# Optimization experiments

Measured on AMD Instinct MI355X. Metric: run time of the kernel, lower is better.

The kernel has to match this reference:

```python
import jax, jax.numpy as jnp
import numpy as np

D_MODEL, D_STATE, EXPAND, D_CONV, HEADDIM = 1024, 128, 2, 4, 64
D_INNER = EXPAND * D_MODEL                      # 2048
NHEADS = D_INNER // HEADDIM                     # 32
NGROUPS = 1
CONV_DIM = D_INNER + 2 * NGROUPS * D_STATE      # 2304
D_IN_PROJ = 2 * D_INNER + 2 * NGROUPS * D_STATE + NHEADS  # 4384
BATCH, SEQ = 2, 4096
EPS = 1e-5


def setup_inputs() -> dict:
    key = jax.random.key(0)
    ks = jax.random.split(key, 6)
    sn = lambda k, shape, sc: jax.random.normal(k, shape, jnp.float32) * sc
    # dt_bias such that softplus(dt_bias) spans [1e-3, 0.1] (mamba2 init)
    dt = jnp.linspace(1e-3, 0.1, NHEADS)
    return {
        "x": sn(ks[0], (BATCH, SEQ, D_MODEL), 1.0),
        "ln_w": jnp.ones((D_MODEL,), jnp.float32),
        "ln_b": jnp.zeros((D_MODEL,), jnp.float32),
        "in_proj_w": sn(ks[1], (D_IN_PROJ, D_MODEL), D_MODEL ** -0.5),
        "conv_w": sn(ks[2], (CONV_DIM, D_CONV), D_CONV ** -0.5),
        "conv_b": jnp.zeros((CONV_DIM,), jnp.float32),
        "dt_bias": jnp.log(jnp.expm1(dt)).astype(jnp.float32),
        "A_log": jnp.log(jnp.arange(1, NHEADS + 1, dtype=jnp.float32)),
        "D": jnp.ones((NHEADS,), jnp.float32),
        "norm_w": jnp.ones((D_INNER,), jnp.float32),
        "out_proj_w": sn(ks[3], (D_MODEL, D_INNER), D_INNER ** -0.5),
    }


def _mamba2(u, in_proj_w, conv_w, conv_b, dt_bias, A_log, Dp, norm_w, out_proj_w):
    b, l, _ = u.shape
    zxbcdt = u @ in_proj_w.T                              # [b,l,4384]
    z, xBC, dt = jnp.split(zxbcdt, [D_INNER, D_INNER + CONV_DIM], axis=-1)
    # causal depthwise conv1d over channels, then SiLU
    xBC = jnp.transpose(xBC, (0, 2, 1))                   # [b,conv_dim,l]
    xBC = jax.lax.conv_general_dilated(
        xBC, conv_w[:, None, :], window_strides=(1,),
        padding=[(D_CONV - 1, 0)], feature_group_count=CONV_DIM,
        dimension_numbers=("NCH", "OIH", "NCH"))
    xBC = jax.nn.silu(jnp.transpose(xBC, (0, 2, 1)) + conv_b)
    x, Bm, Cm = jnp.split(xBC, [D_INNER, D_INNER + NGROUPS * D_STATE], axis=-1)
    dt = jax.nn.softplus(dt + dt_bias)                    # [b,l,h]
    A = -jnp.exp(A_log)                                   # [h]
    xh = x.reshape(b, l, NHEADS, HEADDIM)
    # time-major for the selective scan
    dt_t, x_t = jnp.moveaxis(dt, 1, 0), jnp.moveaxis(xh, 1, 0)
    B_t, C_t = jnp.moveaxis(Bm, 1, 0), jnp.moveaxis(Cm, 1, 0)

    def step(h, inputs):
        dtk, xk, Bk, Ck = inputs                          # [b,h],[b,h,p],[b,n],[b,n]
        decay = jnp.exp(dtk * A)                          # [b,h]
        h = h * decay[:, :, None, None] + (dtk[:, :, None, None] * xk[..., None]) * Bk[:, None, None, :]
        y = jnp.einsum("bhpn,bn->bhp", h, Ck)
        return h, y

    h0 = jnp.zeros((b, NHEADS, HEADDIM, D_STATE), u.dtype)
    _, ys = jax.lax.scan(step, h0, (dt_t, x_t, B_t, C_t))  # ys: [l,b,h,p]
    y = jnp.moveaxis(ys, 0, 1) + Dp[None, None, :, None] * xh
    y = y.reshape(b, l, D_INNER)
    # gated RMSNorm: rmsnorm(y * silu(z)) * norm_w
    y = y * jax.nn.silu(z)
    y = y * jax.lax.rsqrt(jnp.mean(y * y, axis=-1, keepdims=True) + EPS) * norm_w
    return y @ out_proj_w.T


def reference(x, ln_w, ln_b, in_proj_w, conv_w, conv_b, dt_bias, A_log, D, norm_w, out_proj_w):
    mu = jnp.mean(x, -1, keepdims=True)
    var = jnp.mean((x - mu) ** 2, -1, keepdims=True)
    xn = (x - mu) * jax.lax.rsqrt(var + EPS) * ln_w + ln_b
    # dropout is identity at inference
    return x + _mamba2(xn, in_proj_w, conv_w, conv_b, dt_bias, A_log, D, norm_w, out_proj_w)
```

## Files before the change

kernel.cpp:

```cpp
#include <hip/hip_runtime.h>
#include <cstdint>

#define D_MODEL 1024
#define D_INNER 2048
#define NHEADS 32
#define HEADDIM 64
#define D_STATE 128
#define CONV_DIM 2304
#define D_IN_PROJ 4384
#define SEQ 4096
#define NROWS 8192
#define NPROJ_PAD 4480
#define TCH 128
#define NCHUNK 32
#define CR 8

typedef float f32x4 __attribute__((ext_vector_type(4)));
typedef __bf16 bf16x8 __attribute__((ext_vector_type(8)));
typedef unsigned short u16;

__device__ __forceinline__ u16 f2bf(float f) {
  uint32_t u = __builtin_bit_cast(uint32_t, f);
  u += 0x7FFFu + ((u >> 16) & 1u);
  return (u16)(u >> 16);
}
__device__ __forceinline__ float bf2f(u16 h) {
  return __builtin_bit_cast(float, (uint32_t)h << 16);
}
__device__ __forceinline__ float dexp(float a) { return expf(fminf(0.f, a)); }
__device__ __forceinline__ int sw(int v) { return (((v & 7) ^ ((v >> 3) & 7)) << 3); }

typedef __attribute__((address_space(1))) const void gv_t;
typedef __attribute__((address_space(3))) void lv_t;
__device__ __forceinline__ void gload_lds16(const void* g, void* l) {
  __builtin_amdgcn_global_load_lds((gv_t*)g, (lv_t*)l, 16, 0, 0);
}

__global__ __launch_bounds__(256) void cvt_pad(const float* __restrict__ s,
                                               u16* __restrict__ d, int n_src, int n_dst) {
  int i = (blockIdx.x * 256 + threadIdx.x) * 4;
  int stride = gridDim.x * 256 * 4;
  for (; i < n_dst; i += stride) {
    ushort4 o;
    if (i < n_src) {
      float4 v = *(const float4*)&s[i];
      o.x = f2bf(v.x); o.y = f2bf(v.y); o.z = f2bf(v.z); o.w = f2bf(v.w);
    } else {
      o.x = o.y = o.z = o.w = 0;
    }
    *(ushort4*)&d[i] = o;
  }
}

__global__ __launch_bounds__(256) void cvt_w2s(const float* __restrict__ s,
                                               const float* __restrict__ nw,
                                               u16* __restrict__ d, int n) {
  int i = (blockIdx.x * 256 + threadIdx.x) * 4;
  int stride = gridDim.x * 256 * 4;
  for (; i < n; i += stride) {
    float4 v = *(const float4*)&s[i];
    int c = i & (D_INNER - 1);
    ushort4 o;
    o.x = f2bf(v.x * nw[c]);
    o.y = f2bf(v.y * nw[c + 1]);
    o.z = f2bf(v.z * nw[c + 2]);
    o.w = f2bf(v.w * nw[c + 3]);
    *(ushort4*)&d[i] = o;
  }
}

__global__ __launch_bounds__(256) void ln_kernel(const float* __restrict__ x,
                                                 const float* __restrict__ w,
                                                 const float* __restrict__ b,
                                                 u16* __restrict__ out) {
  int row = blockIdx.x, tid = threadIdx.x;
  const float4 v = *(const float4*)&x[(long)row * D_MODEL + tid * 4];
  float s1 = v.x + v.y + v.z + v.w;
  float s2 = v.x * v.x + v.y * v.y + v.z * v.z + v.w * v.w;
#pragma unroll
  for (int m = 32; m >= 1; m >>= 1) {
    s1 += __shfl_xor(s1, m);
    s2 += __shfl_xor(s2, m);
  }
  __shared__ float p1[4], p2[4];
  if ((tid & 63) == 0) { p1[tid >> 6] = s1; p2[tid >> 6] = s2; }
  __syncthreads();
  s1 = p1[0] + p1[1] + p1[2] + p1[3];
  s2 = p2[0] + p2[1] + p2[2] + p2[3];
  float mean = s1 * (1.f / D_MODEL);
  float var = s2 * (1.f / D_MODEL) - mean * mean;
  float rstd = rsqrtf(var + 1e-5f);
  const float4 wv = *(const float4*)&w[tid * 4];
  const float4 bv = *(const float4*)&b[tid * 4];
  ushort4 o;
  o.x = f2bf((v.x - mean) * rstd * wv.x + bv.x);
  o.y = f2bf((v.y - mean) * rstd * wv.y + bv.y);
  o.z = f2bf((v.z - mean) * rstd * wv.z + bv.z);
  o.w = f2bf((v.w - mean) * rstd * wv.w + bv.w);
  *(ushort4*)&out[(long)row * D_MODEL + tid * 4] = o;
}

template <int MODE>
__global__ __launch_bounds__(256, 4) void gemm_bt(const u16* __restrict__ A,
                                                  const u16* __restrict__ B, int K,
                                                  u16* __restrict__ zb,
                                                  u16* __restrict__ xb,
                                                  float* __restrict__ dtb,
                                                  float* __restrict__ C,
                                                  const float* __restrict__ resid,
                                                  const float* __restrict__ rvec) {
  __shared__ __align__(16) u16 As[128 * 64];
  __shared__ __align__(16) u16 Bs[128 * 64];
  const int tid = threadIdx.x;
  int m0, n0;
  if (MODE == 0) {
    const int k = (blockIdx.x & 7) * 280 + (blockIdx.x >> 3);
    const int st = k / 40, inner = k % 40;
    m0 = ((st & 7) * 8 + (inner & 7)) * 128;
    n0 = ((st >> 3) * 5 + (inner >> 3)) * 128;
  } else {
    const int wg = (blockIdx.x & 7) * 64 + (blockIdx.x >> 3);
    m0 = (wg & 63) * 128;
    n0 = (wg >> 6) * 128;
  }
  const int w = tid >> 6, l = tid & 63;
  const int wm = w >> 1, wn = w & 1;

  f32x4 acc[4][4] = {};

  for (int k0 = 0; k0 < K; k0 += 64) {
#pragma unroll
    for (int i = 0; i < 4; ++i) {
      int idx = i * 256 + tid;
      int row = idx >> 3, slot = idx & 7;
      int ks = slot ^ (row & 7);
      const u16* ga = A + (long)(m0 + row) * K + k0 + ks * 8;
      gload_lds16(ga, (char*)As + idx * 16);
      const u16* gb = B + (long)(n0 + row) * K + k0 + ks * 8;
      gload_lds16(gb, (char*)Bs + idx * 16);
    }
    __syncthreads();
    bf16x8 af[2][4], bfr[2][4];
#pragma unroll
    for (int kk = 0; kk < 2; ++kk)
#pragma unroll
      for (int f = 0; f < 4; ++f) {
        int rowa = wm * 64 + f * 16 + (l & 15);
        int ca = ((kk << 2) | (l >> 4)) ^ (rowa & 7);
        af[kk][f] = *(const bf16x8*)((const char*)As + rowa * 128 + ca * 16);
        int rowb = wn * 64 + f * 16 + (l & 15);
        int cb2 = ((kk << 2) | (l >> 4)) ^ (rowb & 7);
        bfr[kk][f] = *(const bf16x8*)((const char*)Bs + rowb * 128 + cb2 * 16);
      }
#pragma unroll
    for (int kk = 0; kk < 2; ++kk)
#pragma unroll
      for (int mf = 0; mf < 4; ++mf)
#pragma unroll
        for (int nf = 0; nf < 4; ++nf)
          acc[mf][nf] = __builtin_amdgcn_mfma_f32_16x16x32_bf16(
              af[kk][mf], bfr[kk][nf], acc[mf][nf], 0, 0, 0);
    __syncthreads();
  }
#pragma unroll
  for (int mf = 0; mf < 4; ++mf)
#pragma unroll
    for (int nf = 0; nf < 4; ++nf) {
      int col = n0 + wn * 64 + nf * 16 + (l & 15);
#pragma unroll
      for (int r = 0; r < 4; ++r) {
        int rowm = m0 + wm * 64 + mf * 16 + (l >> 4) * 4 + r;
        float v = acc[mf][nf][r];
        if (MODE == 0) {
          if (col < D_INNER)
            zb[(long)rowm * D_INNER + col] = f2bf(v);
          else if (col < D_INNER + CONV_DIM)
            xb[(long)rowm * CONV_DIM + (col - D_INNER)] = f2bf(v);
          else if (col < D_IN_PROJ)
            dtb[(long)rowm * NHEADS + (col - D_INNER - CONV_DIM)] = v;
        } else {
          long off = (long)rowm * D_MODEL + col;
          C[off] = v * rvec[rowm] + resid[off];
        }
      }
    }
}

__global__ __launch_bounds__(256) void conv_silu_kernel(const u16* __restrict__ xr,
                                                        const float* __restrict__ cw,
                                                        const float* __restrict__ cb,
                                                        u16* __restrict__ xp,
                                                        u16* __restrict__ bc) {
  const int c = blockIdx.x * 256 + threadIdx.x;
  const int row0 = blockIdx.y * CR;
  const int t0 = row0 & (SEQ - 1);
  const float4 wv = *(const float4*)&cw[c * 4];
  const float bias = cb[c];
  float xwin[CR + 3];
#pragma unroll
  for (int k = 0; k < CR + 3; ++k) {
    int t = t0 - 3 + k;
    xwin[k] = (t >= 0) ? bf2f(xr[(long)(row0 - 3 + k) * CONV_DIM + c]) : 0.f;
  }
#pragma unroll
  for (int j = 0; j < CR; ++j) {
    float a = bias + xwin[j] * wv.x + xwin[j + 1] * wv.y + xwin[j + 2] * wv.z +
              xwin[j + 3] * wv.w;
    a = a / (1.f + expf(-a));
    int row = row0 + j;
    if (c < D_INNER)
      xp[(long)row * D_INNER + c] = f2bf(a);
    else
      bc[(long)row * (2 * D_STATE) + (c - D_INNER)] = f2bf(a);
  }
}

__global__ __launch_bounds__(256, 3) void ssd_state_kernel(
    const u16* __restrict__ xp, const u16* __restrict__ bcb,
    const float* __restrict__ dtf, const float* __restrict__ dt_bias,
    const float* __restrict__ A_log, u16* __restrict__ S,
    float* __restrict__ cdk) {
  const int hh = blockIdx.x, cc = blockIdx.y, bb = blockIdx.z;
  const int tid = threadIdx.x, w = tid >> 6, l = tid & 63;
  __shared__ __align__(16) u16 BT[128 * 128];
  __shared__ __align__(16) u16 WXT[64 * 128];
  __shared__ float ws[128];
  const long rowbase = (long)bb * SEQ + cc * TCH;
  const float Ah = -expf(A_log[hh]);
  const float dbias = dt_bias[hh];

#pragma unroll
  for (int i = 0; i < 8; ++i) {
    int slot = i * 256 + tid, t = slot >> 4, nb = slot & 15;
    bf16x8 v = *(const bf16x8*)&bcb[(rowbase + t) * 256 + nb * 8];
    const u16* e = (const u16*)&v;
#pragma unroll
    for (int j = 0; j < 8; ++j) {
      int n = nb * 8 + j;
      BT[n * 128 + (t ^ sw(n))] = e[j];
    }
  }
  if (w == 0) {
    float r0 = dtf[(rowbase + l) * NHEADS + hh] + dbias;
    float r1 = dtf[(rowbase + 64 + l) * NHEADS + hh] + dbias;
    float d0 = r0 > 20.f ? r0 : log1pf(expf(r0));
    float d1 = r1 > 20.f ? r1 : log1pf(expf(r1));
    float a0 = d0 * Ah, a1 = d1 * Ah;
#pragma unroll
    for (int d = 1; d < 64; d <<= 1) { float u = __shfl_up(a0, d); if (l >= d) a0 += u; }
#pragma unroll
    for (int d = 1; d < 64; d <<= 1) { float u = __shfl_up(a1, d); if (l >= d) a1 += u; }
    float t0 = __shfl(a0, 63);
    float tot = __shfl(a1, 63) + t0;
    ws[l] = dexp(tot - a0) * d0;
    ws[64 + l] = dexp(tot - (a1 + t0)) * d1;
    if (l == 0) cdk[(bb * 32 + hh) * NCHUNK + cc] = dexp(tot);
  }
  __syncthreads();
#pragma unroll
  for (int i = 0; i < 4; ++i) {
    int slot = i * 256 + tid, t = slot >> 3, pb = slot & 7;
    bf16x8 v = *(const bf16x8*)&xp[(rowbase + t) * D_INNER + hh * 64 + pb * 8];
    float wt = ws[t];
    const u16* e = (const u16*)&v;
#pragma unroll
    for (int j = 0; j < 8; ++j) {
      int p = pb * 8 + j;
      WXT[p * 128 + (t ^ sw(p))] = f2bf(bf2f(e[j]) * wt);
    }
  }
  __syncthreads();

  f32x4 acc[8] = {};
  const int p = w * 16 + (l & 15);
  const int swp = sw(p);
#pragma unroll
  for (int kc = 0; kc < 4; ++kc) {
    int tsl = kc * 32 + (l >> 4) * 8;
    bf16x8 af = *(const bf16x8*)&WXT[p * 128 + (tsl ^ swp)];
#pragma unroll
    for (int nt = 0; nt < 8; ++nt) {
      int n = nt * 16 + (l & 15);
      bf16x8 bfv = *(const bf16x8*)&BT[n * 128 + (tsl ^ sw(n))];
      acc[nt] = __builtin_amdgcn_mfma_f32_16x16x32_bf16(af, bfv, acc[nt], 0, 0, 0);
    }
  }
  u16* Sb = S + ((long)(bb * 32 + hh) * NCHUNK + cc) * 8192;
#pragma unroll
  for (int nt = 0; nt < 8; ++nt)
#pragma unroll
    for (int r = 0; r < 4; ++r) {
      int prow = w * 16 + (l >> 4) * 4 + r;
      Sb[prow * 128 + nt * 16 + (l & 15)] = f2bf(acc[nt][r]);
    }
}

__global__ __launch_bounds__(256) void ssd_combine(u16* __restrict__ SH,
                                                   const float* __restrict__ cdk) {
  const int hh = blockIdx.y, bb = blockIdx.z;
  const int pp = blockIdx.x * 16 + (threadIdx.x >> 4);
  const int nn = (threadIdx.x & 15) * 8;
  const int bh = bb * 32 + hh;
  u16* base = SH + (long)bh * NCHUNK * 8192 + pp * 128 + nn;
  const float* ck = cdk + bh * NCHUNK;
  float h[8] = {};
  for (int c = 0; c < NCHUNK; ++c) {
    bf16x8 sv = *(bf16x8*)(base + (long)c * 8192);
    const u16* se = (const u16*)&sv;
    u16 o[8];
#pragma unroll
    for (int j = 0; j < 8; ++j) o[j] = f2bf(h[j]);
    *(bf16x8*)(base + (long)c * 8192) = *(bf16x8*)o;
    float d = ck[c];
#pragma unroll
    for (int j = 0; j < 8; ++j) h[j] = fmaf(h[j], d, bf2f(se[j]));
  }
}

__global__ __launch_bounds__(256, 2) void ssd_y_kernel(
    const u16* __restrict__ xp, const u16* __restrict__ bcb,
    const float* __restrict__ dtf, const float* __restrict__ dt_bias,
    const float* __restrict__ A_log, const float* __restrict__ Dp,
    const u16* __restrict__ H, u16* __restrict__ zb,
    float* __restrict__ psum) {
  const int hh = blockIdx.x, cc = blockIdx.y, bb = blockIdx.z;
  const int tid = threadIdx.x, w = tid >> 6, l = tid & 63;
  __shared__ __align__(16) u16 Cs[128 * 128];
  __shared__ __align__(16) u16 XT[64 * 128];
  __shared__ __align__(16) u16 Bp[32 * 128];
  __shared__ __align__(16) u16 Ms[128 * 40];
  __shared__ float sig[128], dts[128], esg[128];
  const long rowbase = (long)bb * SEQ + cc * TCH;
  const float Ah = -expf(A_log[hh]);
  const float Dh = Dp[hh];
  const float dbias = dt_bias[hh];

#pragma unroll
  for (int i = 0; i < 8; ++i) {
    int idx = i * 256 + tid, t = idx >> 4, sl = idx & 15;
    gload_lds16(bcb + (rowbase + t) * 256 + 128 + ((sl ^ (t & 15)) * 8),
                (char*)Cs + idx * 16);
  }
  if (w == 0) {
    float r0 = dtf[(rowbase + l) * NHEADS + hh] + dbias;
    float r1 = dtf[(rowbase + 64 + l) * NHEADS + hh] + dbias;
    float d0 = r0 > 20.f ? r0 : log1pf(expf(r0));
    float d1 = r1 > 20.f ? r1 : log1pf(expf(r1));
    float a0 = d0 * Ah, a1 = d1 * Ah;
#pragma unroll
    for (int d = 1; d < 64; d <<= 1) { float u = __shfl_up(a0, d); if (l >= d) a0 += u; }
#pragma unroll
    for (int d = 1; d < 64; d <<= 1) { float u = __shfl_up(a1, d); if (l >= d) a1 += u; }
    float t0 = __shfl(a0, 63);
    sig[l] = a0; sig[64 + l] = a1 + t0;
    dts[l] = d0; dts[64 + l] = d1;
    esg[l] = dexp(a0); esg[64 + l] = dexp(a1 + t0);
  }
#pragma unroll
  for (int i = 0; i < 4; ++i) {
    int slot = i * 256 + tid, t = slot >> 3, pb = slot & 7;
    bf16x8 v = *(const bf16x8*)&xp[(rowbase + t) * D_INNER + hh * 64 + pb * 8];
    const u16* e = (const u16*)&v;
#pragma unroll
    for (int j = 0; j < 8; ++j) {
      int p = pb * 8 + j;
      XT[p * 128 + (t ^ sw(p))] = e[j];
    }
  }
  __syncthreads();

  bf16x8 cfr[2][4];
#pragma unroll
  for (int tt = 0; tt < 2; ++tt) {
    int t = (w * 2 + tt) * 16 + (l & 15);
#pragma unroll
    for (int kc = 0; kc < 4; ++kc) {
      int sl = (kc * 4 + (l >> 4)) ^ (t & 15);
      cfr[tt][kc] = *(const bf16x8*)&Cs[t * 128 + sl * 8];
    }
  }
  f32x4 y1[2][4] = {};

  for (int sp = 0; sp < 4; ++sp) {
    __syncthreads();
#pragma unroll
    for (int i = 0; i < 2; ++i) {
      int idx = i * 256 + tid, sr = idx >> 4, sl = idx & 15;
      gload_lds16(bcb + (rowbase + sp * 32 + sr) * 256 + ((sl ^ (sr & 15)) * 8),
                  (char*)Bp + idx * 16);
    }
    __syncthreads();
    f32x4 g[2][2] = {};
#pragma unroll
    for (int st = 0; st < 2; ++st)
#pragma unroll
      for (int kc = 0; kc < 4; ++kc) {
        int s = st * 16 + (l & 15);
        int sl = (kc * 4 + (l >> 4)) ^ (s & 15);
        bf16x8 bfv = *(const bf16x8*)&Bp[s * 128 + sl * 8];
        g[0][st] = __builtin_amdgcn_mfma_f32_16x16x32_bf16(cfr[0][kc], bfv, g[0][st], 0, 0, 0);
        g[1][st] = __builtin_amdgcn_mfma_f32_16x16x32_bf16(cfr[1][kc], bfv, g[1][st], 0, 0, 0);
      }
#pragma unroll
    for (int tt = 0; tt < 2; ++tt)
#pragma unroll
      for (int st = 0; st < 2; ++st)
#pragma unroll
        for (int r = 0; r < 4; ++r) {
          int t = (w * 2 + tt) * 16 + (l >> 4) * 4 + r;
          int s = sp * 32 + st * 16 + (l & 15);
          float m = 0.f;
          if (s <= t) m = g[tt][st][r] * dexp(sig[t] - sig[s]) * dts[s];
          Ms[t * 40 + st * 16 + (l & 15)] = f2bf(m);
        }
    __syncthreads();
#pragma unroll
    for (int tt = 0; tt < 2; ++tt) {
      int t = (w * 2 + tt) * 16 + (l & 15);
      bf16x8 mf = *(const bf16x8*)&Ms[t * 40 + (l >> 4) * 8];
#pragma unroll
      for (int pt = 0; pt < 4; ++pt) {
        int p = pt * 16 + (l & 15);
        int ssl = sp * 32 + (l >> 4) * 8;
        bf16x8 xf = *(const bf16x8*)&XT[p * 128 + (ssl ^ sw(p))];
        y1[tt][pt] = __builtin_amdgcn_mfma_f32_16x16x32_bf16(mf, xf, y1[tt][pt], 0, 0, 0);
      }
    }
  }
  f32x4 y2[2][4] = {};
  const u16* Hb = H + ((long)(bb * 32 + hh) * NCHUNK + cc) * 8192;
#pragma unroll
  for (int pt = 0; pt < 4; ++pt) {
    int p = pt * 16 + (l & 15);
#pragma unroll
    for (int kc = 0; kc < 4; ++kc) {
      bf16x8 hf = *(const bf16x8*)&Hb[p * 128 + kc * 32 + (l >> 4) * 8];
      y2[0][pt] = __builtin_amdgcn_mfma_f32_16x16x32_bf16(cfr[0][kc], hf, y2[0][pt], 0, 0, 0);
      y2[1][pt] = __builtin_amdgcn_mfma_f32_16x16x32_bf16(cfr[1][kc], hf, y2[1][pt], 0, 0, 0);
    }
  }
  float s2[2][4] = {};
#pragma unroll
  for (int tt = 0; tt < 2; ++tt)
#pragma unroll
    for (int pt = 0; pt < 4; ++pt)
#pragma unroll
      for (int r = 0; r < 4; ++r) {
        int t = (w * 2 + tt) * 16 + (l >> 4) * 4 + r;
        int p = pt * 16 + (l & 15);
        float xv = bf2f(XT[p * 128 + (t ^ sw(p))]);
        float yv = y1[tt][pt][r] + esg[t] * y2[tt][pt][r] + Dh * xv;
        long off = (rowbase + t) * (long)D_INNER + hh * 64 + p;
        float zv = bf2f(zb[off]);
        float gg = yv * (zv / (1.f + expf(-zv)));
        zb[off] = f2bf(gg);
        s2[tt][r] += gg * gg;
      }
#pragma unroll
  for (int tt = 0; tt < 2; ++tt)
#pragma unroll
    for (int r = 0; r < 4; ++r) {
      float v = s2[tt][r];
      v += __shfl_xor(v, 1);
      v += __shfl_xor(v, 2);
      v += __shfl_xor(v, 4);
      v += __shfl_xor(v, 8);
      if ((l & 15) == 0) {
        int t = (w * 2 + tt) * 16 + (l >> 4) * 4 + r;
        psum[(rowbase + t) * NHEADS + hh] = v;
      }
    }
}

__global__ __launch_bounds__(256) void r_reduce(const float* __restrict__ psum,
                                                float* __restrict__ rvec) {
  int row = blockIdx.x * 256 + threadIdx.x;
  const float4* p = (const float4*)&psum[(long)row * NHEADS];
  float s = 0.f;
#pragma unroll
  for (int i = 0; i < 8; ++i) {
    float4 v = p[i];
    s += v.x + v.y + v.z + v.w;
  }
  rvec[row] = rsqrtf(s * (1.f / D_INNER) + 1e-5f);
}

extern "C" void kernel_launch(void* const* d_in, const int* in_sizes, int n_in,
                              void* d_out, int out_size, void* d_ws, size_t ws_size,
                              hipStream_t stream) {
  const float* x = (const float*)d_in[0];
  const float* ln_w = (const float*)d_in[1];
  const float* ln_b = (const float*)d_in[2];
  const float* in_proj_w = (const float*)d_in[3];
  const float* conv_w = (const float*)d_in[4];
  const float* conv_b = (const float*)d_in[5];
  const float* dt_bias = (const float*)d_in[6];
  const float* A_log = (const float*)d_in[7];
  const float* Dvec = (const float*)d_in[8];
  const float* norm_w = (const float*)d_in[9];
  const float* out_proj_w = (const float*)d_in[10];
  float* out = (float*)d_out;

  char* ws = (char*)d_ws;
  u16* W2bf = (u16*)(ws + 0);
  u16* zbf = (u16*)(ws + 4194304);
  u16* xpart = (u16*)(ws + 37748736);
  u16* bcbf = (u16*)(ws + 71303168);
  float* dtf = (float*)(ws + 75497472);
  float* cdk = (float*)(ws + 76546048);
  u16* W1bf = (u16*)(ws + 76554240);
  u16* xbcraw = (u16*)(ws + 85729280);
  u16* SH = (u16*)(ws + 76554240);
  float* psum = (float*)(ws + 110108672);
  float* rvec = (float*)(ws + 111157248);
  u16* xnbf = (u16*)d_out;

  cvt_pad<<<512, 256, 0, stream>>>(in_proj_w, W1bf, D_IN_PROJ * D_MODEL,
                                   NPROJ_PAD * D_MODEL);
  cvt_w2s<<<512, 256, 0, stream>>>(out_proj_w, norm_w, W2bf, D_MODEL * D_INNER);
  ln_kernel<<<NROWS, 256, 0, stream>>>(x, ln_w, ln_b, xnbf);
  gemm_bt<0><<<35 * 64, 256, 0, stream>>>(xnbf, W1bf, D_MODEL, zbf, xbcraw, dtf,
                                          nullptr, nullptr, nullptr);
  conv_silu_kernel<<<dim3(9, NROWS / CR), 256, 0, stream>>>(xbcraw, conv_w, conv_b,
                                                            xpart, bcbf);
  ssd_state_kernel<<<dim3(32, NCHUNK, 2), 256, 0, stream>>>(xpart, bcbf, dtf, dt_bias,
                                                            A_log, SH, cdk);
  ssd_combine<<<dim3(4, 32, 2), 256, 0, stream>>>(SH, cdk);
  ssd_y_kernel<<<dim3(32, NCHUNK, 2), 256, 0, stream>>>(xpart, bcbf, dtf, dt_bias,
                                                        A_log, Dvec, SH, zbf, psum);
  r_reduce<<<32, 256, 0, stream>>>(psum, rvec);
  gemm_bt<1><<<8 * 64, 256, 0, stream>>>(zbf, W2bf, D_INNER, nullptr, nullptr,
                                         nullptr, out, x, rvec);
}
```

Baseline: 295.6 us.

## Load C/B fragments directly from global and compute full mask in one pass

The ssd_y kernel no longer stages C and B tiles in shared memory. MFMA fragments are read straight from global memory, and the four-step loop over B slices becomes a single pass that computes the full 128x128 masked CB matrix into a wider Ms buffer. This removes several __syncthreads and shrinks shared-memory use, and the launch bounds are raised to 3 blocks per CU to get more occupancy. The trade-offs are uncoalesced-ish global fragment loads, more accumulator registers (g[2][8]), and possible spills under the tighter register budget.

```diff
diff --git a/kernel.cpp b/kernel.cpp
--- a/kernel.cpp
+++ b/kernel.cpp
@@ -317,7 +317,7 @@
   }
 }
 
-__global__ __launch_bounds__(256, 2) void ssd_y_kernel(
+__global__ __launch_bounds__(256, 3) void ssd_y_kernel(
     const u16* __restrict__ xp, const u16* __restrict__ bcb,
     const float* __restrict__ dtf, const float* __restrict__ dt_bias,
     const float* __restrict__ A_log, const float* __restrict__ Dp,
@@ -325,22 +325,14 @@
     float* __restrict__ psum) {
   const int hh = blockIdx.x, cc = blockIdx.y, bb = blockIdx.z;
   const int tid = threadIdx.x, w = tid >> 6, l = tid & 63;
-  __shared__ __align__(16) u16 Cs[128 * 128];
   __shared__ __align__(16) u16 XT[64 * 128];
-  __shared__ __align__(16) u16 Bp[32 * 128];
-  __shared__ __align__(16) u16 Ms[128 * 40];
+  __shared__ __align__(16) u16 Ms[128 * 136];
   __shared__ float sig[128], dts[128], esg[128];
   const long rowbase = (long)bb * SEQ + cc * TCH;
   const float Ah = -expf(A_log[hh]);
   const float Dh = Dp[hh];
   const float dbias = dt_bias[hh];
 
-#pragma unroll
-  for (int i = 0; i < 8; ++i) {
-    int idx = i * 256 + tid, t = idx >> 4, sl = idx & 15;
-    gload_lds16(bcb + (rowbase + t) * 256 + 128 + ((sl ^ (t & 15)) * 8),
-                (char*)Cs + idx * 16);
-  }
   if (w == 0) {
     float r0 = dtf[(rowbase + l) * NHEADS + hh] + dbias;
     float r1 = dtf[(rowbase + 64 + l) * NHEADS + hh] + dbias;
@@ -374,57 +366,49 @@
   for (int tt = 0; tt < 2; ++tt) {
     int t = (w * 2 + tt) * 16 + (l & 15);
 #pragma unroll
+    for (int kc = 0; kc < 4; ++kc)
+      cfr[tt][kc] = *(const bf16x8*)&bcb[(rowbase + t) * 256 + 128 + kc * 32 +
+                                         (l >> 4) * 8];
+  }
+  f32x4 g[2][8] = {};
+#pragma unroll
+  for (int st = 0; st < 8; ++st) {
+    int s = st * 16 + (l & 15);
+#pragma unroll
     for (int kc = 0; kc < 4; ++kc) {
-      int sl = (kc * 4 + (l >> 4)) ^ (t & 15);
-      cfr[tt][kc] = *(const bf16x8*)&Cs[t * 128 + sl * 8];
-    }
-  }
+      bf16x8 bfv = *(const bf16x8*)&bcb[(rowbase + s) * 256 + kc * 32 + (l >> 4) * 8];
+      g[0][st] = __builtin_amdgcn_mfma_f32_16x16x32_bf16(cfr[0][kc], bfv, g[0][st], 0, 0, 0);
+      g[1][st] = __builtin_amdgcn_mfma_f32_16x16x32_bf16(cfr[1][kc], bfv, g[1][st], 0, 0, 0);
+    }
+  }
+#pragma unroll
+  for (int tt = 0; tt < 2; ++tt)
+#pragma unroll
+    for (int st = 0; st < 8; ++st)
+#pragma unroll
+      for (int r = 0; r < 4; ++r) {
+        int t = (w * 2 + tt) * 16 + (l >> 4) * 4 + r;
+        int s = st * 16 + (l & 15);
+        float m = 0.f;
+        if (s <= t) m = g[tt][st][r] * dexp(sig[t] - sig[s]) * dts[s];
+        Ms[t * 136 + s] = f2bf(m);
+      }
+  __syncthreads();
+
   f32x4 y1[2][4] = {};
-
-  for (int sp = 0; sp < 4; ++sp) {
-    __syncthreads();
-#pragma unroll
-    for (int i = 0; i < 2; ++i) {
-      int idx = i * 256 + tid, sr = idx >> 4, sl = idx & 15;
-      gload_lds16(bcb + (rowbase + sp * 32 + sr) * 256 + ((sl ^ (sr & 15)) * 8),
-                  (char*)Bp + idx * 16);
-    }
-    __syncthreads();
-    f32x4 g[2][2] = {};
-#pragma unroll
-    for (int st = 0; st < 2; ++st)
-#pragma unroll
-      for (int kc = 0; kc < 4; ++kc) {
-        int s = st * 16 + (l & 15);
-        int sl = (kc * 4 + (l >> 4)) ^ (s & 15);
-        bf16x8 bfv = *(const bf16x8*)&Bp[s * 128 + sl * 8];
-        g[0][st] = __builtin_amdgcn_mfma_f32_16x16x32_bf16(cfr[0][kc], bfv, g[0][st], 0, 0, 0);
-        g[1][st] = __builtin_amdgcn_mfma_f32_16x16x32_bf16(cfr[1][kc], bfv, g[1][st], 0, 0, 0);
-      }
-#pragma unroll
-    for (int tt = 0; tt < 2; ++tt)
-#pragma unroll
-      for (int st = 0; st < 2; ++st)
-#pragma unroll
-        for (int r = 0; r < 4; ++r) {
-          int t = (w * 2 + tt) * 16 + (l >> 4) * 4 + r;
-          int s = sp * 32 + st * 16 + (l & 15);
-          float m = 0.f;
-          if (s <= t) m = g[tt][st][r] * dexp(sig[t] - sig[s]) * dts[s];
-          Ms[t * 40 + st * 16 + (l & 15)] = f2bf(m);
-        }
-    __syncthreads();
-#pragma unroll
-    for (int tt = 0; tt < 2; ++tt) {
-      int t = (w * 2 + tt) * 16 + (l & 15);
-      bf16x8 mf = *(const bf16x8*)&Ms[t * 40 + (l >> 4) * 8];
-#pragma unroll
-      for (int pt = 0; pt < 4; ++pt) {
-        int p = pt * 16 + (l & 15);
-        int ssl = sp * 32 + (l >> 4) * 8;
-        bf16x8 xf = *(const bf16x8*)&XT[p * 128 + (ssl ^ sw(p))];
-        y1[tt][pt] = __builtin_amdgcn_mfma_f32_16x16x32_bf16(mf, xf, y1[tt][pt], 0, 0, 0);
-      }
+#pragma unroll
+  for (int kc = 0; kc < 4; ++kc) {
+    int t0r = (w * 2) * 16 + (l & 15);
+    int t1r = (w * 2 + 1) * 16 + (l & 15);
+    bf16x8 mf0 = *(const bf16x8*)&Ms[t0r * 136 + kc * 32 + (l >> 4) * 8];
+    bf16x8 mf1 = *(const bf16x8*)&Ms[t1r * 136 + kc * 32 + (l >> 4) * 8];
+#pragma unroll
+    for (int pt = 0; pt < 4; ++pt) {
+      int p = pt * 16 + (l & 15);
+      int ssl = kc * 32 + (l >> 4) * 8;
+      bf16x8 xf = *(const bf16x8*)&XT[p * 128 + (ssl ^ sw(p))];
+      y1[0][pt] = __builtin_amdgcn_mfma_f32_16x16x32_bf16(mf0, xf, y1[0][pt], 0, 0, 0);
+      y1[1][pt] = __builtin_amdgcn_mfma_f32_16x16x32_bf16(mf1, xf, y1[1][pt], 0, 0, 0);
     }
   }
   f32x4 y2[2][4] = {};
```

Measured after the change: 301.2 us. No clear change (+1.9%).
